# Kernel tuning notes

Hardware: AMD Instinct MI355X
Metric: run time of the kernel (lower is better)

## Reference

```python
import jax, jax.numpy as jnp
import numpy as np
import math

B, S, D = 4, 2048, 1024

def setup_inputs() -> dict:
    key = jax.random.key(0)
    k1, k2, k3, k4 = jax.random.split(key, 4)
    scale = 1.0 / math.sqrt(D)
    return {
        "x": jax.random.normal(k1, (B, S, D), dtype=jnp.float32),
        "w_q": jax.random.normal(k2, (D, D), dtype=jnp.float32) * scale,
        "w_k": jax.random.normal(k3, (D, D), dtype=jnp.float32) * scale,
        "w_v": jax.random.normal(k4, (D, D), dtype=jnp.float32) * scale,
        "causal": 1,
    }

def reference(x, w_q, w_k, w_v, causal):
    # QKV projections: nn.Linear(dim, dim, bias=False) -> x @ W.T
    q = jnp.einsum('bsd,ed->bse', x, w_q)
    k = jnp.einsum('bsd,ed->bse', x, w_k)
    v = jnp.einsum('bsd,ed->bse', x, w_v)
    d_k = q.shape[-1]
    scores = jnp.einsum('bqd,bkd->bqk', q, k) / jnp.sqrt(jnp.asarray(d_k, q.dtype))
    if causal:
        seq_len = q.shape[-2]
        mask = jnp.triu(jnp.ones((seq_len, seq_len), dtype=bool), k=1)
        scores = jnp.where(mask, jnp.asarray(-jnp.inf, scores.dtype), scores)
    weights = jax.nn.softmax(scores, axis=-1)
    return jnp.einsum('bqk,bkd->bqd', weights, v)
```

## Files before the change

kernel.cpp:

```cpp
#include <hip/hip_runtime.h>
#include <stdint.h>

typedef unsigned short u16;
typedef __attribute__((ext_vector_type(8))) __bf16 bf16x8;
typedef __attribute__((ext_vector_type(4))) float f32x4;

__device__ __forceinline__ u16 f2bf(float f) {
  unsigned u = __float_as_uint(f);
  u += 0x7FFF + ((u >> 16) & 1);
  return (u16)(u >> 16);
}

__device__ __forceinline__ float bf2f(u16 h) {
  return __uint_as_float(((unsigned)h) << 16);
}

__device__ __forceinline__ void llds16(const u16* g, u16* l) {
  __builtin_amdgcn_global_load_lds(
      (const __attribute__((address_space(1))) void*)g,
      (__attribute__((address_space(3))) void*)l, 16, 0, 0);
}

__global__ __launch_bounds__(256) void cast_all(
    const float* __restrict__ x, const float* __restrict__ wq,
    const float* __restrict__ wk, const float* __restrict__ wv,
    u16* __restrict__ xb, u16* __restrict__ wb, float* __restrict__ lsum,
    int* __restrict__ cnt) {
  int i = blockIdx.x * 256 + threadIdx.x;
  if (i < 8192) lsum[i] = 0.f;
  if (i < 2) cnt[i] = 0;
  const float* src; u16* dst; int off;
  if (i < 2097152)      { src = x;  dst = xb;            off = i; }
  else if (i < 2359296) { src = wq; dst = wb;            off = i - 2097152; }
  else if (i < 2621440) { src = wk; dst = wb + 1048576;  off = i - 2359296; }
  else                  { src = wv; dst = wb + 2097152;  off = i - 2621440; }
  float4 f = ((const float4*)src)[off];
  ushort4 o;
  o.x = f2bf(f.x); o.y = f2bf(f.y); o.z = f2bf(f.z); o.w = f2bf(f.w);
  ((ushort4*)dst)[off] = o;
}

template<int MODE>
__global__ __launch_bounds__(256) void gemm_nt(
    const u16* __restrict__ A, long long sA, int lda,
    const u16* __restrict__ B, long long sB, int ldb,
    void* __restrict__ Cp, long long sC, int ldc,
    int K, u16* __restrict__ vt, float scale,
    float* __restrict__ lsum, const int* __restrict__ causalp) {
  const int t = threadIdx.x;
  const int causal = (MODE == 0) ? 1 : causalp[0];

  int rt = blockIdx.x, ct = blockIdx.y;

  const int rowbase = rt * 128;
  const int colbase = ct * 128;
  const u16* Ab = A + (long long)blockIdx.z * sA;
  const u16* Bb = B + (long long)blockIdx.z * sB;

  int Keff = K;
  if (MODE == 2 && causal) Keff = min(K, rowbase + 128);

  __shared__ u16 As[8192];
  __shared__ u16 Bs[8192];

  const int lane = t & 63;
  const int wv = t >> 6;
  const int wr = wv >> 1;
  const int wc = wv & 1;
  const int quad = lane >> 4;
  const int lr = lane & 15;

  f32x4 acc[4][4];
  const f32x4 zero = {0.f, 0.f, 0.f, 0.f};
#pragma unroll
  for (int i = 0; i < 4; ++i)
#pragma unroll
    for (int j = 0; j < 4; ++j) acc[i][j] = zero;

  {
    const int csw = (t & 7) ^ ((t >> 3) & 7);
    const u16* ga = Ab + (long long)(rowbase + (t >> 3)) * lda + csw * 8;
    const u16* gb = Bb + (long long)(colbase + (t >> 3)) * ldb + csw * 8;
    const long long ra = 32LL * lda, rb = 32LL * ldb;
    u16* la = As + t * 8;
    u16* lb = Bs + t * 8;

    const int m7 = lr & 7;
    const int a_base = (wr * 64 + lr) * 64 + ((quad ^ m7) * 8);
    const int b_base = (wc * 64 + lr) * 64 + ((quad ^ m7) * 8);

    for (int k0 = 0; k0 < Keff; k0 += 64) {
      __syncthreads();
#pragma unroll
      for (int i = 0; i < 4; ++i) {
        llds16(ga + k0 + i * ra, la + i * 2048);
        llds16(gb + k0 + i * rb, lb + i * 2048);
      }
      __syncthreads();
#pragma unroll
      for (int ks = 0; ks < 2; ++ks) {
        const int ko = ks ? 32 : 0;
        bf16x8 af[4], bfv[4];
#pragma unroll
        for (int tm = 0; tm < 4; ++tm)
          af[tm] = *(const bf16x8*)(As + ((a_base + tm * 1024) ^ ko));
#pragma unroll
        for (int tn = 0; tn < 4; ++tn)
          bfv[tn] = *(const bf16x8*)(Bs + ((b_base + tn * 1024) ^ ko));
#pragma unroll
        for (int tm = 0; tm < 4; ++tm)
#pragma unroll
          for (int tn = 0; tn < 4; ++tn)
            acc[tm][tn] = __builtin_amdgcn_mfma_f32_16x16x32_bf16(
                af[tm], bfv[tn], acc[tm][tn], 0, 0, 0);
      }
    }
  }

  if (MODE == 0 && colbase >= 2048) {
#pragma unroll
    for (int tm = 0; tm < 4; ++tm) {
      int s0 = rowbase + wr * 64 + tm * 16 + quad * 4;
      int b = s0 >> 11;
      int sl = s0 & 2047;
#pragma unroll
      for (int tn = 0; tn < 4; ++tn) {
        int e = colbase - 2048 + wc * 64 + tn * 16 + lr;
        ushort4 o;
        o.x = f2bf(acc[tm][tn][0]);
        o.y = f2bf(acc[tm][tn][1]);
        o.z = f2bf(acc[tm][tn][2]);
        o.w = f2bf(acc[tm][tn][3]);
        *(ushort4*)(vt + ((long long)(b * 1024 + e)) * 2048 + sl) = o;
      }
    }
    return;
  }

#pragma unroll
  for (int tm = 0; tm < 4; ++tm) {
#pragma unroll
    for (int r = 0; r < 4; ++r) {
      const int grow = rowbase + wr * 64 + tm * 16 + quad * 4 + r;
      float li, rsum = 0.f;
      if (MODE == 2) li = __builtin_amdgcn_rcpf(lsum[blockIdx.z * 2048 + grow]);
#pragma unroll
      for (int tn = 0; tn < 4; ++tn) {
        const int gcol = colbase + wc * 64 + tn * 16 + lr;
        float val = acc[tm][tn][r];
        if (MODE == 0) {
          ((u16*)Cp)[(long long)grow * ldc + gcol] = f2bf(val);
        } else if (MODE == 1) {
          u16* C = (u16*)Cp + (long long)blockIdx.z * sC;
          float ex = (causal && gcol > grow) ? 0.f : __expf(val * scale);
          C[(long long)grow * ldc + gcol] = f2bf(ex);
          rsum += ex;
        } else {
          float* C = (float*)Cp + (long long)blockIdx.z * sC;
          C[(long long)grow * ldc + gcol] = val * li;
        }
      }
      if (MODE == 1) {
#pragma unroll
        for (int o = 8; o > 0; o >>= 1) rsum += __shfl_xor(rsum, o, 64);
        if (lr == 0)
          atomicAdd(&lsum[blockIdx.z * 2048 + grow], rsum);
      }
    }
  }
}

template<int MODE>
__device__ __forceinline__ void gemm_core(
    int rt, int ct, int zb, int causal, u16* As, u16* Bs,
    const u16* __restrict__ A, long long sA, int lda,
    const u16* __restrict__ B, long long sB, int ldb,
    void* __restrict__ Cp, long long sC, int ldc,
    int K, float scale, float* __restrict__ lsum) {
  const int t = threadIdx.x;

  const int rowbase = rt * 128;
  const int colbase = ct * 128;
  const u16* Ab = A + (long long)zb * sA;
  const u16* Bb = B + (long long)zb * sB;

  int Keff = K;
  if (MODE == 2 && causal) Keff = min(K, rowbase + 128);

  const int lane = t & 63;
  const int wv = t >> 6;
  const int wr = wv >> 1;
  const int wc = wv & 1;
  const int quad = lane >> 4;
  const int lr = lane & 15;

  f32x4 acc[4][4];
  const f32x4 zero = {0.f, 0.f, 0.f, 0.f};
#pragma unroll
  for (int i = 0; i < 4; ++i)
#pragma unroll
    for (int j = 0; j < 4; ++j) acc[i][j] = zero;

  {
    const int csw = (t & 7) ^ ((t >> 3) & 7);
    const u16* ga = Ab + (long long)(rowbase + (t >> 3)) * lda + csw * 8;
    const u16* gb = Bb + (long long)(colbase + (t >> 3)) * ldb + csw * 8;
    const long long ra = 32LL * lda, rb = 32LL * ldb;
    u16* la = As + t * 8;
    u16* lb = Bs + t * 8;

    const int m7 = lr & 7;
    const int a_base = (wr * 64 + lr) * 64 + ((quad ^ m7) * 8);
    const int b_base = (wc * 64 + lr) * 64 + ((quad ^ m7) * 8);

#pragma unroll
    for (int i = 0; i < 4; ++i) {
      llds16(ga + i * ra, la + i * 2048);
      llds16(gb + i * rb, lb + i * 2048);
    }
    __syncthreads();
    for (int k0 = 0; k0 < Keff; k0 += 64) {
      const int nb = ((k0 >> 6) & 1) ^ 1;
      const int bo = (nb ^ 1) << 13;
      if (k0 + 64 < Keff) {
#pragma unroll
        for (int i = 0; i < 4; ++i) {
          llds16(ga + (k0 + 64) + i * ra, la + nb * 8192 + i * 2048);
          llds16(gb + (k0 + 64) + i * rb, lb + nb * 8192 + i * 2048);
        }
      }
#pragma unroll
      for (int ks = 0; ks < 2; ++ks) {
        const int ko = ks ? 32 : 0;
        bf16x8 af[4], bfv[4];
#pragma unroll
        for (int tm = 0; tm < 4; ++tm)
          af[tm] = *(const bf16x8*)(As + bo + ((a_base + tm * 1024) ^ ko));
#pragma unroll
        for (int tn = 0; tn < 4; ++tn)
          bfv[tn] = *(const bf16x8*)(Bs + bo + ((b_base + tn * 1024) ^ ko));
#pragma unroll
        for (int tm = 0; tm < 4; ++tm)
#pragma unroll
          for (int tn = 0; tn < 4; ++tn)
            acc[tm][tn] = __builtin_amdgcn_mfma_f32_16x16x32_bf16(
                af[tm], bfv[tn], acc[tm][tn], 0, 0, 0);
      }
      __syncthreads();
    }
  }

#pragma unroll
  for (int tm = 0; tm < 4; ++tm) {
#pragma unroll
    for (int r = 0; r < 4; ++r) {
      const int grow = rowbase + wr * 64 + tm * 16 + quad * 4 + r;
      float li, rsum = 0.f;
      if (MODE == 2) li = __builtin_amdgcn_rcpf(lsum[zb * 2048 + grow]);
#pragma unroll
      for (int tn = 0; tn < 4; ++tn) {
        const int gcol = colbase + wc * 64 + tn * 16 + lr;
        float val = acc[tm][tn][r];
        if (MODE == 1) {
          u16* C = (u16*)Cp + (long long)zb * sC;
          float ex = (causal && gcol > grow) ? 0.f : __expf(val * scale);
          C[(long long)grow * ldc + gcol] = f2bf(ex);
          rsum += ex;
        } else {
          float* C = (float*)Cp + (long long)zb * sC;
          C[(long long)grow * ldc + gcol] = val * li;
        }
      }
      if (MODE == 1) {
#pragma unroll
        for (int o = 8; o > 0; o >>= 1) rsum += __shfl_xor(rsum, o, 64);
        if (lr == 0)
          atomicAdd(&lsum[zb * 2048 + grow], rsum);
      }
    }
  }
}

__global__ __launch_bounds__(256) void gemm_sc(
    const u16* __restrict__ qk, u16* __restrict__ sb,
    float* __restrict__ lsum, const int* __restrict__ causalp,
    int* __restrict__ cnt) {
  __shared__ u16 As[16384];
  __shared__ u16 Bs[16384];
  __shared__ int jsh;
  const int causal = causalp[0];
  const int njobs = causal ? 544 : 1024;
  for (;;) {
    if (threadIdx.x == 0) jsh = atomicAdd(cnt, 1);
    __syncthreads();
    const int j = jsh;
    if (j >= njobs) return;
    int zb, rt, ct;
    if (causal) {
      zb = j / 136;
      int i2 = j - zb * 136, r = 0;
      while (i2 >= r + 1) { i2 -= r + 1; ++r; }
      rt = r; ct = i2;
    } else {
      zb = j >> 8;
      const int rem = j & 255;
      rt = rem >> 4; ct = rem & 15;
    }
    gemm_core<1>(rt, ct, zb, causal, As, Bs,
                 qk, 2048LL * 2048, 2048, qk + 1024, 2048LL * 2048, 2048,
                 sb, 2048LL * 2048, 2048, 1024, 0.03125f, lsum);
    __syncthreads();
  }
}

__global__ __launch_bounds__(256) void gemm_pv(
    const u16* __restrict__ sb, const u16* __restrict__ vtb,
    float* __restrict__ out, float* __restrict__ lsum,
    const int* __restrict__ causalp, int* __restrict__ cnt) {
  __shared__ u16 As[16384];
  __shared__ u16 Bs[16384];
  __shared__ int jsh;
  const int causal = causalp[0];
  for (;;) {
    if (threadIdx.x == 0) jsh = atomicAdd(cnt, 1);
    __syncthreads();
    const int j = jsh;
    if (j >= 512) return;
    const int rt = 15 - (j >> 5);
    const int rem = j & 31;
    const int zb = rem >> 3;
    const int ct = rem & 7;
    gemm_core<2>(rt, ct, zb, causal, As, Bs,
                 sb, 2048LL * 2048, 2048, vtb, 1024LL * 2048, 2048,
                 out, 2048LL * 1024, 1024, 2048, 1.0f, lsum);
    __syncthreads();
  }
}

extern "C" void kernel_launch(void* const* d_in, const int* in_sizes, int n_in,
                              void* d_out, int out_size, void* d_ws, size_t ws_size,
                              hipStream_t stream) {
  const float* x  = (const float*)d_in[0];
  const float* wq = (const float*)d_in[1];
  const float* wk = (const float*)d_in[2];
  const float* wv = (const float*)d_in[3];
  const int* causal = (const int*)d_in[4];
  float* out = (float*)d_out;

  char* ws = (char*)d_ws;
  u16* xb = (u16*)(ws);
  u16* wb = (u16*)(ws + 16777216);
  u16* qk = (u16*)(ws + 23068672);
  u16* vt = (u16*)(ws + 56623104);
  u16* sb = (u16*)(ws + 73400320);
  float* lsum = (float*)(ws + 106954752);
  int* cnt = (int*)(ws + 106987520);

  cast_all<<<11264, 256, 0, stream>>>(x, wq, wk, wv, xb, wb, lsum, cnt);

  gemm_nt<0><<<dim3(64, 24, 1), 256, 0, stream>>>(
      xb, 0, 1024, wb, 0, 1024, qk, 0, 2048, 1024, vt, 1.0f, nullptr, causal);

  gemm_sc<<<dim3(512, 1, 1), 256, 0, stream>>>(qk, sb, lsum, causal, cnt);

  gemm_pv<<<dim3(512, 1, 1), 256, 0, stream>>>(sb, vt, out, lsum, causal,
                                               cnt + 1);
}
```

Measured before the change: 237.1 us.

## Use 512-thread blocks with static tile mapping instead of atomic work queues

New measurement: 239.9 us. About the same (+1.2%).

```diff
diff --git a/kernel.cpp b/kernel.cpp
--- a/kernel.cpp
+++ b/kernel.cpp
@@ -24,11 +24,9 @@
 __global__ __launch_bounds__(256) void cast_all(
     const float* __restrict__ x, const float* __restrict__ wq,
     const float* __restrict__ wk, const float* __restrict__ wv,
-    u16* __restrict__ xb, u16* __restrict__ wb, float* __restrict__ lsum,
-    int* __restrict__ cnt) {
+    u16* __restrict__ xb, u16* __restrict__ wb, float* __restrict__ lsum) {
   int i = blockIdx.x * 256 + threadIdx.x;
   if (i < 8192) lsum[i] = 0.f;
-  if (i < 2) cnt[i] = 0;
   const float* src; u16* dst; int off;
   if (i < 2097152)      { src = x;  dst = xb;            off = i; }
   else if (i < 2359296) { src = wq; dst = wb;            off = i - 2097152; }
@@ -171,7 +169,7 @@
 }
 
 template<int MODE>
-__device__ __forceinline__ void gemm_core(
+__device__ __forceinline__ void gemm_core8(
     int rt, int ct, int zb, int causal, u16* As, u16* Bs,
     const u16* __restrict__ A, long long sA, int lda,
     const u16* __restrict__ B, long long sB, int ldb,
@@ -189,34 +187,34 @@
 
   const int lane = t & 63;
   const int wv = t >> 6;
-  const int wr = wv >> 1;
-  const int wc = wv & 1;
+  const int wr = wv >> 2;
+  const int wc = wv & 3;
   const int quad = lane >> 4;
   const int lr = lane & 15;
 
-  f32x4 acc[4][4];
+  f32x4 acc[4][2];
   const f32x4 zero = {0.f, 0.f, 0.f, 0.f};
 #pragma unroll
   for (int i = 0; i < 4; ++i)
 #pragma unroll
-    for (int j = 0; j < 4; ++j) acc[i][j] = zero;
+    for (int j = 0; j < 2; ++j) acc[i][j] = zero;
 
   {
     const int csw = (t & 7) ^ ((t >> 3) & 7);
     const u16* ga = Ab + (long long)(rowbase + (t >> 3)) * lda + csw * 8;
     const u16* gb = Bb + (long long)(colbase + (t >> 3)) * ldb + csw * 8;
-    const long long ra = 32LL * lda, rb = 32LL * ldb;
+    const long long ra = 64LL * lda, rb = 64LL * ldb;
     u16* la = As + t * 8;
     u16* lb = Bs + t * 8;
 
     const int m7 = lr & 7;
     const int a_base = (wr * 64 + lr) * 64 + ((quad ^ m7) * 8);
-    const int b_base = (wc * 64 + lr) * 64 + ((quad ^ m7) * 8);
-
-#pragma unroll
-    for (int i = 0; i < 4; ++i) {
-      llds16(ga + i * ra, la + i * 2048);
-      llds16(gb + i * rb, lb + i * 2048);
+    const int b_base = (wc * 32 + lr) * 64 + ((quad ^ m7) * 8);
+
+#pragma unroll
+    for (int i = 0; i < 2; ++i) {
+      llds16(ga + i * ra, la + i * 4096);
+      llds16(gb + i * rb, lb + i * 4096);
     }
     __syncthreads();
     for (int k0 = 0; k0 < Keff; k0 += 64) {
@@ -224,25 +222,25 @@
       const int bo = (nb ^ 1) << 13;
       if (k0 + 64 < Keff) {
 #pragma unroll
-        for (int i = 0; i < 4; ++i) {
-          llds16(ga + (k0 + 64) + i * ra, la + nb * 8192 + i * 2048);
-          llds16(gb + (k0 + 64) + i * rb, lb + nb * 8192 + i * 2048);
+        for (int i = 0; i < 2; ++i) {
+          llds16(ga + (k0 + 64) + i * ra, la + nb * 8192 + i * 4096);
+          llds16(gb + (k0 + 64) + i * rb, lb + nb * 8192 + i * 4096);
         }
       }
 #pragma unroll
       for (int ks = 0; ks < 2; ++ks) {
         const int ko = ks ? 32 : 0;
-        bf16x8 af[4], bfv[4];
+        bf16x8 af[4], bfv[2];
 #pragma unroll
         for (int tm = 0; tm < 4; ++tm)
           af[tm] = *(const bf16x8*)(As + bo + ((a_base + tm * 1024) ^ ko));
 #pragma unroll
-        for (int tn = 0; tn < 4; ++tn)
+        for (int tn = 0; tn < 2; ++tn)
           bfv[tn] = *(const bf16x8*)(Bs + bo + ((b_base + tn * 1024) ^ ko));
 #pragma unroll
         for (int tm = 0; tm < 4; ++tm)
 #pragma unroll
-          for (int tn = 0; tn < 4; ++tn)
+          for (int tn = 0; tn < 2; ++tn)
             acc[tm][tn] = __builtin_amdgcn_mfma_f32_16x16x32_bf16(
                 af[tm], bfv[tn], acc[tm][tn], 0, 0, 0);
       }
@@ -258,8 +256,8 @@
       float li, rsum = 0.f;
       if (MODE == 2) li = __builtin_amdgcn_rcpf(lsum[zb * 2048 + grow]);
 #pragma unroll
-      for (int tn = 0; tn < 4; ++tn) {
-        const int gcol = colbase + wc * 64 + tn * 16 + lr;
+      for (int tn = 0; tn < 2; ++tn) {
+        const int gcol = colbase + wc * 32 + tn * 16 + lr;
         float val = acc[tm][tn][r];
         if (MODE == 1) {
           u16* C = (u16*)Cp + (long long)zb * sC;
@@ -281,60 +279,45 @@
   }
 }
 
-__global__ __launch_bounds__(256) void gemm_sc(
+__global__ __launch_bounds__(512) void gemm_sc(
     const u16* __restrict__ qk, u16* __restrict__ sb,
-    float* __restrict__ lsum, const int* __restrict__ causalp,
-    int* __restrict__ cnt) {
+    float* __restrict__ lsum, const int* __restrict__ causalp) {
   __shared__ u16 As[16384];
   __shared__ u16 Bs[16384];
-  __shared__ int jsh;
   const int causal = causalp[0];
-  const int njobs = causal ? 544 : 1024;
-  for (;;) {
-    if (threadIdx.x == 0) jsh = atomicAdd(cnt, 1);
-    __syncthreads();
-    const int j = jsh;
-    if (j >= njobs) return;
-    int zb, rt, ct;
-    if (causal) {
-      zb = j / 136;
-      int i2 = j - zb * 136, r = 0;
-      while (i2 >= r + 1) { i2 -= r + 1; ++r; }
-      rt = r; ct = i2;
-    } else {
-      zb = j >> 8;
-      const int rem = j & 255;
-      rt = rem >> 4; ct = rem & 15;
-    }
-    gemm_core<1>(rt, ct, zb, causal, As, Bs,
-                 qk, 2048LL * 2048, 2048, qk + 1024, 2048LL * 2048, 2048,
-                 sb, 2048LL * 2048, 2048, 1024, 0.03125f, lsum);
-    __syncthreads();
-  }
-}
-
-__global__ __launch_bounds__(256) void gemm_pv(
+  const int j = blockIdx.x;
+  int zb, rt, ct;
+  if (causal) {
+    if (j >= 544) return;
+    zb = j / 136;
+    int i2 = j - zb * 136, r = 0;
+    while (i2 >= r + 1) { i2 -= r + 1; ++r; }
+    rt = r; ct = i2;
+  } else {
+    zb = j >> 8;
+    const int rem = j & 255;
+    rt = rem >> 4; ct = rem & 15;
+  }
+  gemm_core8<1>(rt, ct, zb, causal, As, Bs,
+                qk, 2048LL * 2048, 2048, qk + 1024, 2048LL * 2048, 2048,
+                sb, 2048LL * 2048, 2048, 1024, 0.03125f, lsum);
+}
+
+__global__ __launch_bounds__(512) void gemm_pv(
     const u16* __restrict__ sb, const u16* __restrict__ vtb,
     float* __restrict__ out, float* __restrict__ lsum,
-    const int* __restrict__ causalp, int* __restrict__ cnt) {
+    const int* __restrict__ causalp) {
   __shared__ u16 As[16384];
   __shared__ u16 Bs[16384];
-  __shared__ int jsh;
   const int causal = causalp[0];
-  for (;;) {
-    if (threadIdx.x == 0) jsh = atomicAdd(cnt, 1);
-    __syncthreads();
-    const int j = jsh;
-    if (j >= 512) return;
-    const int rt = 15 - (j >> 5);
-    const int rem = j & 31;
-    const int zb = rem >> 3;
-    const int ct = rem & 7;
-    gemm_core<2>(rt, ct, zb, causal, As, Bs,
-                 sb, 2048LL * 2048, 2048, vtb, 1024LL * 2048, 2048,
-                 out, 2048LL * 1024, 1024, 2048, 1.0f, lsum);
-    __syncthreads();
-  }
+  const int s = ((blockIdx.x & 7) << 6) + (blockIdx.x >> 3);
+  const int zb = s >> 7;
+  const int ct = (s & 127) >> 4;
+  const int m = s & 15;
+  const int rt = (s & 32) ? m : 15 - m;
+  gemm_core8<2>(rt, ct, zb, causal, As, Bs,
+                sb, 2048LL * 2048, 2048, vtb, 1024LL * 2048, 2048,
+                out, 2048LL * 1024, 1024, 2048, 1.0f, lsum);
 }
 
 extern "C" void kernel_launch(void* const* d_in, const int* in_sizes, int n_in,
@@ -354,15 +337,13 @@
   u16* vt = (u16*)(ws + 56623104);
   u16* sb = (u16*)(ws + 73400320);
   float* lsum = (float*)(ws + 106954752);
-  int* cnt = (int*)(ws + 106987520);
-
-  cast_all<<<11264, 256, 0, stream>>>(x, wq, wk, wv, xb, wb, lsum, cnt);
+
+  cast_all<<<11264, 256, 0, stream>>>(x, wq, wk, wv, xb, wb, lsum);
 
   gemm_nt<0><<<dim3(64, 24, 1), 256, 0, stream>>>(
       xb, 0, 1024, wb, 0, 1024, qk, 0, 2048, 1024, vt, 1.0f, nullptr, causal);
 
-  gemm_sc<<<dim3(512, 1, 1), 256, 0, stream>>>(qk, sb, lsum, causal, cnt);
-
-  gemm_pv<<<dim3(512, 1, 1), 256, 0, stream>>>(sb, vt, out, lsum, causal,
-                                               cnt + 1);
-}
+  gemm_sc<<<dim3(1024, 1, 1), 512, 0, stream>>>(qk, sb, lsum, causal);
+
+  gemm_pv<<<dim3(512, 1, 1), 512, 0, stream>>>(sb, vt, out, lsum, causal);
+}
```

## Replace atomic work-queue scheduling with static XCD-aware tile mapping

Applied to the files above, without the earlier changes.

Result: faster. 231.3 us (-2.4%).

```diff
diff --git a/kernel.cpp b/kernel.cpp
--- a/kernel.cpp
+++ b/kernel.cpp
@@ -24,11 +24,9 @@
 __global__ __launch_bounds__(256) void cast_all(
     const float* __restrict__ x, const float* __restrict__ wq,
     const float* __restrict__ wk, const float* __restrict__ wv,
-    u16* __restrict__ xb, u16* __restrict__ wb, float* __restrict__ lsum,
-    int* __restrict__ cnt) {
+    u16* __restrict__ xb, u16* __restrict__ wb, float* __restrict__ lsum) {
   int i = blockIdx.x * 256 + threadIdx.x;
   if (i < 8192) lsum[i] = 0.f;
-  if (i < 2) cnt[i] = 0;
   const float* src; u16* dst; int off;
   if (i < 2097152)      { src = x;  dst = xb;            off = i; }
   else if (i < 2359296) { src = wq; dst = wb;            off = i - 2097152; }
@@ -283,58 +281,44 @@
 
 __global__ __launch_bounds__(256) void gemm_sc(
     const u16* __restrict__ qk, u16* __restrict__ sb,
-    float* __restrict__ lsum, const int* __restrict__ causalp,
-    int* __restrict__ cnt) {
+    float* __restrict__ lsum, const int* __restrict__ causalp) {
   __shared__ u16 As[16384];
   __shared__ u16 Bs[16384];
-  __shared__ int jsh;
   const int causal = causalp[0];
-  const int njobs = causal ? 544 : 1024;
-  for (;;) {
-    if (threadIdx.x == 0) jsh = atomicAdd(cnt, 1);
-    __syncthreads();
-    const int j = jsh;
-    if (j >= njobs) return;
-    int zb, rt, ct;
-    if (causal) {
-      zb = j / 136;
-      int i2 = j - zb * 136, r = 0;
-      while (i2 >= r + 1) { i2 -= r + 1; ++r; }
-      rt = r; ct = i2;
-    } else {
-      zb = j >> 8;
-      const int rem = j & 255;
-      rt = rem >> 4; ct = rem & 15;
-    }
-    gemm_core<1>(rt, ct, zb, causal, As, Bs,
-                 qk, 2048LL * 2048, 2048, qk + 1024, 2048LL * 2048, 2048,
-                 sb, 2048LL * 2048, 2048, 1024, 0.03125f, lsum);
-    __syncthreads();
-  }
+  const int zb = blockIdx.z;
+  const int xcd = blockIdx.x & 7;
+  const int chunk = ((blockIdx.x >> 3) + 8 * blockIdx.z) & 31;
+  int rt, ct;
+  if (chunk < 17) {
+    int i2 = xcd * 17 + chunk, c = 0;
+    while (i2 >= 16 - c) { i2 -= 16 - c; ++c; }
+    ct = c; rt = c + i2;
+  } else {
+    if (causal) return;
+    int i2 = xcd * 15 + (chunk - 17), r = 0;
+    while (i2 >= r + 1) { i2 -= r + 1; ++r; }
+    rt = i2; ct = r + 1;
+  }
+  gemm_core<1>(rt, ct, zb, causal, As, Bs,
+               qk, 2048LL * 2048, 2048, qk + 1024, 2048LL * 2048, 2048,
+               sb, 2048LL * 2048, 2048, 1024, 0.03125f, lsum);
 }
 
 __global__ __launch_bounds__(256) void gemm_pv(
     const u16* __restrict__ sb, const u16* __restrict__ vtb,
     float* __restrict__ out, float* __restrict__ lsum,
-    const int* __restrict__ causalp, int* __restrict__ cnt) {
+    const int* __restrict__ causalp) {
   __shared__ u16 As[16384];
   __shared__ u16 Bs[16384];
-  __shared__ int jsh;
   const int causal = causalp[0];
-  for (;;) {
-    if (threadIdx.x == 0) jsh = atomicAdd(cnt, 1);
-    __syncthreads();
-    const int j = jsh;
-    if (j >= 512) return;
-    const int rt = 15 - (j >> 5);
-    const int rem = j & 31;
-    const int zb = rem >> 3;
-    const int ct = rem & 7;
-    gemm_core<2>(rt, ct, zb, causal, As, Bs,
-                 sb, 2048LL * 2048, 2048, vtb, 1024LL * 2048, 2048,
-                 out, 2048LL * 1024, 1024, 2048, 1.0f, lsum);
-    __syncthreads();
-  }
+  const int s = ((blockIdx.x & 7) << 6) + (blockIdx.x >> 3);
+  const int zb = s >> 7;
+  const int ct = (s & 127) >> 4;
+  const int m = s & 15;
+  const int rt = (s & 32) ? m : 15 - m;
+  gemm_core<2>(rt, ct, zb, causal, As, Bs,
+               sb, 2048LL * 2048, 2048, vtb, 1024LL * 2048, 2048,
+               out, 2048LL * 1024, 1024, 2048, 1.0f, lsum);
 }
 
 extern "C" void kernel_launch(void* const* d_in, const int* in_sizes, int n_in,
@@ -354,15 +338,13 @@
   u16* vt = (u16*)(ws + 56623104);
   u16* sb = (u16*)(ws + 73400320);
   float* lsum = (float*)(ws + 106954752);
-  int* cnt = (int*)(ws + 106987520);
-
-  cast_all<<<11264, 256, 0, stream>>>(x, wq, wk, wv, xb, wb, lsum, cnt);
+
+  cast_all<<<11264, 256, 0, stream>>>(x, wq, wk, wv, xb, wb, lsum);
 
   gemm_nt<0><<<dim3(64, 24, 1), 256, 0, stream>>>(
       xb, 0, 1024, wb, 0, 1024, qk, 0, 2048, 1024, vt, 1.0f, nullptr, causal);
 
-  gemm_sc<<<dim3(512, 1, 1), 256, 0, stream>>>(qk, sb, lsum, causal, cnt);
-
-  gemm_pv<<<dim3(512, 1, 1), 256, 0, stream>>>(sb, vt, out, lsum, causal,
-                                               cnt + 1);
-}
+  gemm_sc<<<dim3(256, 1, 4), 256, 0, stream>>>(qk, sb, lsum, causal);
+
+  gemm_pv<<<dim3(512, 1, 1), 256, 0, stream>>>(sb, vt, out, lsum, causal);
+}
```
